# Performance work log

Measured on AMD Instinct MI355X. Metric: run time of the kernel, lower is better.

The kernel has to match this reference:

```python
import jax, jax.numpy as jnp
import numpy as np
import math

D_MODEL = 1024
NUM_HEADS = 16
D_K = D_MODEL // NUM_HEADS  # 64
B, S = 4, 2048


def setup_inputs() -> dict:
    key = jax.random.key(0)
    ks = jax.random.split(key, 9)
    sc = 1.0 / math.sqrt(D_MODEL)
    return {
        "x": jax.random.normal(ks[0], (B, S, D_MODEL), jnp.float32),
        "Wq": jax.random.normal(ks[1], (D_MODEL, D_MODEL), jnp.float32) * sc,
        "bq": jax.random.normal(ks[2], (D_MODEL,), jnp.float32) * 0.01,
        "Wk": jax.random.normal(ks[3], (D_MODEL, D_MODEL), jnp.float32) * sc,
        "bk": jax.random.normal(ks[4], (D_MODEL,), jnp.float32) * 0.01,
        "Wv": jax.random.normal(ks[5], (D_MODEL, D_MODEL), jnp.float32) * sc,
        "bv": jax.random.normal(ks[6], (D_MODEL,), jnp.float32) * 0.01,
        "Wo": jax.random.normal(ks[7], (D_MODEL, D_MODEL), jnp.float32) * sc,
        "bo": jax.random.normal(ks[8], (D_MODEL,), jnp.float32) * 0.01,
    }


def reference(x, Wq, bq, Wk, bk, Wv, bv, Wo, bo):
    b, s, d = x.shape
    # Linear projections (torch Linear: x @ W.T + b)
    Q = x @ Wq.T + bq
    K = x @ Wk.T + bk
    V = x @ Wv.T + bv
    # [b, s, h*d_k] -> [b, h, s, d_k]
    split = lambda t: t.reshape(b, s, NUM_HEADS, D_K).transpose(0, 2, 1, 3)
    Q, K, V = split(Q), split(K), split(V)
    # Causal mask: query i can attend to keys j <= i
    seq = jnp.arange(s)
    causal = seq[:, None] >= seq[None, :]  # [s, s]
    # Scaled dot-product attention
    scores = jnp.einsum('bhqd,bhkd->bhqk', Q, K) / math.sqrt(D_K)
    scores = jnp.where(causal, scores, -jnp.inf)
    weights = jax.nn.softmax(scores, axis=-1)
    attn = jnp.einsum('bhqk,bhkd->bhqd', weights, V)
    # [b, h, s, d_v] -> [b, s, h*d_v]
    attn = attn.transpose(0, 2, 1, 3).reshape(b, s, NUM_HEADS * D_K)
    return attn @ Wo.T + bo
```

## Files before the change

kernel.cpp:

```cpp
#include <hip/hip_runtime.h>
#include <hip/hip_bf16.h>


typedef unsigned short u16;
typedef unsigned int u32;
typedef __attribute__((ext_vector_type(2))) unsigned int uint2v;
typedef __attribute__((ext_vector_type(4))) unsigned int uint4v;
typedef __attribute__((ext_vector_type(4))) short short4v;
typedef __attribute__((ext_vector_type(8))) short short8;
typedef __attribute__((ext_vector_type(4))) float f32x4;
typedef __attribute__((ext_vector_type(16))) float f32x16;

#define KDIM   1024
#define S_LEN  2048
#define NHEADS 16
#define DK     64
#define NEG_BIG (-30000.0f)
#define QSCALE 0.18033688011112043f

__device__ __forceinline__ u16 f2bf(float f) {
  unsigned u = __float_as_uint(f);
  return (u16)((u + 0x7FFFu + ((u >> 16) & 1u)) >> 16);
}
__device__ __forceinline__ u32 pkbf(float a, float b) {
  u32 ua = __float_as_uint(a) + 0x8000u;
  u32 ub = __float_as_uint(b) + 0x8000u;
  return __builtin_amdgcn_perm(ub, ua, 0x07060302u);
}
__device__ __forceinline__ void gl_lds16(const u16* g, u16* l) {
  __builtin_amdgcn_global_load_lds((const __attribute__((address_space(1))) void*)g,
                                   (__attribute__((address_space(3))) void*)l, 16, 0, 0);
}

__global__ __launch_bounds__(256) void cvt_kernel(
    const float* __restrict__ x,  const float* __restrict__ Wq,
    const float* __restrict__ Wk, const float* __restrict__ Wv,
    u16* __restrict__ xb, u16* __restrict__ wqb,
    u16* __restrict__ wkb, u16* __restrict__ wvb) {
  const int NX = 2097152, NW = 262144;
  const int total = NX + 3 * NW;
  for (int i = blockIdx.x * 256 + threadIdx.x; i < total; i += gridDim.x * 256) {
    const float* src; u16* dst; int off;
    if (i < NX)               { src = x;  dst = xb;  off = i; }
    else if (i < NX + NW)     { src = Wq; dst = wqb; off = i - NX; }
    else if (i < NX + 2 * NW) { src = Wk; dst = wkb; off = i - NX - NW; }
    else                      { src = Wv; dst = wvb; off = i - NX - 2 * NW; }
    f32x4 v = *(const f32x4*)(src + (size_t)off * 4);
    short4v o;
    o[0] = (short)f2bf(v[0]); o[1] = (short)f2bf(v[1]);
    o[2] = (short)f2bf(v[2]); o[3] = (short)f2bf(v[3]);
    *(short4v*)(dst + (size_t)off * 4) = o;
  }
}

__global__ __launch_bounds__(256) void cvt_wo(const float* __restrict__ W,
                                              u16* __restrict__ out) {
  const int i = blockIdx.x * 256 + threadIdx.x;
  f32x4 v = *(const f32x4*)(W + (size_t)i * 4);
  short4v o;
  o[0] = (short)f2bf(v[0]); o[1] = (short)f2bf(v[1]);
  o[2] = (short)f2bf(v[2]); o[3] = (short)f2bf(v[3]);
  *(short4v*)(out + (size_t)i * 4) = o;
}

template <int MODE>
__device__ __forceinline__ void gemm_body(const u16* __restrict__ A,
                                          const u16* __restrict__ B,
                                          const float* __restrict__ bias,
                                          void* __restrict__ outv) {
  extern __shared__ __align__(16) u16 smem[];
  u16* As0 = smem;
  u16* As1 = smem + 4096;
  u16* Bs0 = smem + 8192;
  u16* Bs1 = smem + 12288;
  const int tid = threadIdx.x;
  const int wave = tid >> 6, lane = tid & 63;
  const int quad = lane >> 4, l16 = lane & 15;
  const int wy = wave >> 1, wx = wave & 1;
  const int m0 = blockIdx.x * 128, n0 = blockIdx.y * 128;

  f32x4 acc[4][4];
#pragma unroll
  for (int i = 0; i < 4; i++)
#pragma unroll
    for (int j = 0; j < 4; j++) acc[i][j] = (f32x4){0.f, 0.f, 0.f, 0.f};

  const int srow = wave * 16 + (lane >> 2);
  const int scol = (lane & 3) * 8;
  const u16* gA0 = A + (size_t)(m0 + srow) * KDIM + scol;
  const u16* gA1 = gA0 + (size_t)64 * KDIM;
  const u16* gB0 = B + (size_t)(n0 + srow) * KDIM + scol;
  const u16* gB1 = gB0 + (size_t)64 * KDIM;
  const int soff = srow * 32 + scol;

  for (int k = 0; k < KDIM; k += 64) {
    __syncthreads();
    gl_lds16(gA0 + k,      &As0[soff]);
    gl_lds16(gA0 + k + 32, &As1[soff]);
    gl_lds16(gA1 + k,      &As0[soff + 2048]);
    gl_lds16(gA1 + k + 32, &As1[soff + 2048]);
    gl_lds16(gB0 + k,      &Bs0[soff]);
    gl_lds16(gB0 + k + 32, &Bs1[soff]);
    gl_lds16(gB1 + k,      &Bs0[soff + 2048]);
    gl_lds16(gB1 + k + 32, &Bs1[soff + 2048]);
    __syncthreads();
#pragma unroll
    for (int h = 0; h < 2; h++) {
      const u16* Ap = h ? As1 : As0;
      const u16* Bp = h ? Bs1 : Bs0;
      short8 af[4], bfr[4];
#pragma unroll
      for (int i = 0; i < 4; i++)
        af[i] = *(const short8*)&Ap[(wy * 64 + i * 16 + l16) * 32 + quad * 8];
#pragma unroll
      for (int j = 0; j < 4; j++)
        bfr[j] = *(const short8*)&Bp[(wx * 64 + j * 16 + l16) * 32 + quad * 8];
#pragma unroll
      for (int i = 0; i < 4; i++)
#pragma unroll
        for (int j = 0; j < 4; j++) {
          if (MODE == 2)
            acc[i][j] = __builtin_amdgcn_mfma_f32_16x16x32_bf16(af[i], bfr[j], acc[i][j], 0, 0, 0);
          else
            acc[i][j] = __builtin_amdgcn_mfma_f32_16x16x32_bf16(bfr[j], af[i], acc[i][j], 0, 0, 0);
        }
    }
  }

  if (MODE == 0 || MODE == 1) {
#pragma unroll
    for (int j = 0; j < 4; j++) {
      const int colb = n0 + wx * 64 + j * 16 + quad * 4;
      const int h = colb >> 6, d0 = colb & 63;
      const f32x4 bv4 = *(const f32x4*)&bias[colb];
#pragma unroll
      for (int i = 0; i < 4; i++) {
        const int row = m0 + wy * 64 + i * 16 + l16;
        const int b = row >> 11, s = row & 2047;
        float v0 = acc[i][j][0] + bv4[0], v1 = acc[i][j][1] + bv4[1];
        float v2 = acc[i][j][2] + bv4[2], v3 = acc[i][j][3] + bv4[3];
        if (MODE == 0) { v0 *= QSCALE; v1 *= QSCALE; v2 *= QSCALE; v3 *= QSCALE; }
        uint2v pk = {pkbf(v0, v1), pkbf(v2, v3)};
        if (MODE == 0) {
          *(uint2v*)&((u16*)outv)[(((size_t)(b * NHEADS + h)) * S_LEN + s) * DK + d0] = pk;
        } else {
          *(uint2v*)&((u16*)outv)[((((size_t)(b * NHEADS + h)) * 32 + (s >> 6)) * 8 +
                                   (d0 >> 3)) * 512 + (s & 63) * 8 + (d0 & 7)] = pk;
        }
      }
    }
  } else if (MODE == 2) {
#pragma unroll
    for (int j = 0; j < 4; j++) {
      const int col = n0 + wx * 64 + j * 16 + l16;
      const int h = col >> 6, d = col & 63;
      const float bvs = bias[col];
#pragma unroll
      for (int i = 0; i < 4; i++) {
        const int rowb = m0 + wy * 64 + i * 16 + quad * 4;
        const int b = rowb >> 11, s0 = rowb & 2047;
        uint2v pk = {pkbf(acc[i][j][0] + bvs, acc[i][j][1] + bvs),
                     pkbf(acc[i][j][2] + bvs, acc[i][j][3] + bvs)};
        *(uint2v*)&((u16*)outv)[((((size_t)(b * NHEADS + h)) * 32 + (s0 >> 6)) * 8 +
                                 ((s0 >> 3) & 7)) * 512 + (size_t)d * 8 + (s0 & 7)] = pk;
      }
    }
  } else {
#pragma unroll
    for (int j = 0; j < 4; j++) {
      const int colb = n0 + wx * 64 + j * 16 + quad * 4;
      const f32x4 bv4 = *(const f32x4*)&bias[colb];
#pragma unroll
      for (int i = 0; i < 4; i++) {
        const int row = m0 + wy * 64 + i * 16 + l16;
        f32x4 v = {acc[i][j][0] + bv4[0], acc[i][j][1] + bv4[1],
                   acc[i][j][2] + bv4[2], acc[i][j][3] + bv4[3]};
        *(f32x4*)&((float*)outv)[(size_t)row * 1024 + colb] = v;
      }
    }
  }
}

__global__ __launch_bounds__(256) void qkv_gemm(
    const u16* __restrict__ xb,
    const u16* __restrict__ wqb, const float* __restrict__ bq,
    const u16* __restrict__ wkb, const float* __restrict__ bk,
    const u16* __restrict__ wvb, const float* __restrict__ bv,
    u16* __restrict__ qb, u16* __restrict__ kb, u16* __restrict__ vb) {
  if (blockIdx.z == 0)      gemm_body<0>(xb, wqb, bq, qb);
  else if (blockIdx.z == 1) gemm_body<1>(xb, wkb, bk, kb);
  else                      gemm_body<2>(xb, wvb, bv, vb);
}

__global__ __launch_bounds__(256) void out_gemm(const u16* __restrict__ A,
                                                const u16* __restrict__ wob,
                                                const float* __restrict__ bo,
                                                float* __restrict__ out) {
  gemm_body<3>(A, wob, bo, out);
}

__global__ __launch_bounds__(256) void attn_kernel(const u16* __restrict__ Qb,
                                                   const u16* __restrict__ Kb,
                                                   const u16* __restrict__ Vb,
                                                   u16* __restrict__ Ob) {
  __shared__ __align__(16) u16 Ks[2][8][512];
  __shared__ __align__(16) u16 Vs[2][8][512];
  const int bh = blockIdx.x;
  const int qt = (int)gridDim.y - 1 - (int)blockIdx.y;
  const int tid = threadIdx.x, wave = tid >> 6, lane = tid & 63;
  const int l32 = lane & 31, hi = lane >> 5;
  const u16* Qh = Qb + (size_t)bh * S_LEN * DK;
  const u16* Kg = Kb + (size_t)bh * S_LEN * DK;
  const u16* Vg = Vb + (size_t)bh * S_LEN * DK;
  const int qw = qt * 128 + wave * 32;
  const int qrow = qw + l32;

  short8 qf[4];
#pragma unroll
  for (int c = 0; c < 4; c++)
    qf[c] = *(const short8*)&Qh[(size_t)qrow * DK + c * 16 + hi * 8];

  short8 ones;
#pragma unroll
  for (int i = 0; i < 8; i++) ones[i] = (short)0x3F80;

  f32x16 zz;
#pragma unroll
  for (int i = 0; i < 16; i++) zz[i] = 0.f;
  f32x16 o0 = zz, o1 = zz, l_acc = zz;

  const int sg = wave * 2;
  const u16* srcK = Kg + sg * 512 + lane * 8;
  const u16* srcV = Vg + sg * 512 + lane * 8;
  u16* dstK0 = &Ks[0][sg][lane * 8];
  u16* dstK1 = &Ks[1][sg][lane * 8];
  u16* dstV0 = &Vs[0][sg][lane * 8];
  u16* dstV1 = &Vs[1][sg][lane * 8];

  for (int t = 0; t <= qt; ++t) {
    const size_t g0 = (size_t)(2 * t) * 4096, g1 = (size_t)(2 * t + 1) * 4096;
    __syncthreads();
    gl_lds16(srcK + g0, dstK0);        gl_lds16(srcK + g0 + 512, dstK0 + 512);
    gl_lds16(srcK + g1, dstK1);        gl_lds16(srcK + g1 + 512, dstK1 + 512);
    gl_lds16(srcV + g0, dstV0);        gl_lds16(srcV + g0 + 512, dstV0 + 512);
    gl_lds16(srcV + g1, dstV1);        gl_lds16(srcV + g1 + 512, dstV1 + 512);
    __syncthreads();

#pragma unroll
    for (int kb = 0; kb < 4; ++kb) {
      const int kbase = t * 128 + kb * 32;
      if (kbase > qw) break;

      f32x16 st = zz;
#pragma unroll
      for (int c = 0; c < 4; c++) {
        const short8 kf = *(const short8*)
            &Ks[kb >> 1][c * 2 + hi][((kb & 1) * 32 + l32) * 8];
        st = __builtin_amdgcn_mfma_f32_32x32x16_bf16(kf, qf[c], st, 0, 0, 0);
      }

      if (kbase == qw) {
#pragma unroll
        for (int r = 0; r < 16; r++) {
          const int ko = (r & 3) + 8 * (r >> 2) + 4 * hi;
          st[r] = (ko > l32) ? NEG_BIG : st[r];
        }
      }

      float e[16];
#pragma unroll
      for (int r = 0; r < 16; r++) e[r] = exp2f(st[r]);

      uint2v sA0 = __builtin_amdgcn_permlane32_swap(pkbf(e[0], e[1]),  pkbf(e[4], e[5]),  false, false);
      uint2v sB0 = __builtin_amdgcn_permlane32_swap(pkbf(e[2], e[3]),  pkbf(e[6], e[7]),  false, false);
      uint2v sA1 = __builtin_amdgcn_permlane32_swap(pkbf(e[8], e[9]),  pkbf(e[12], e[13]), false, false);
      uint2v sB1 = __builtin_amdgcn_permlane32_swap(pkbf(e[10], e[11]), pkbf(e[14], e[15]), false, false);
      union { uint4v u; short8 s; } p0, p1;
      p0.u = (uint4v){sA0[0], sB0[0], sA0[1], sB0[1]};
      p1.u = (uint4v){sA1[0], sB1[0], sA1[1], sB1[1]};
      const short8 pa0 = p0.s, pa1 = p1.s;

      l_acc = __builtin_amdgcn_mfma_f32_32x32x16_bf16(pa0, ones, l_acc, 0, 0, 0);
      l_acc = __builtin_amdgcn_mfma_f32_32x32x16_bf16(pa1, ones, l_acc, 0, 0, 0);

#pragma unroll
      for (int cc = 0; cc < 2; cc++) {
        const int kc = kb * 2 + cc;
        const short8 pa = cc ? pa1 : pa0;
        const short8 vf0 = *(const short8*)&Vs[kc >> 2][(kc & 3) * 2 + hi][l32 * 8];
        const short8 vf1 = *(const short8*)&Vs[kc >> 2][(kc & 3) * 2 + hi][(32 + l32) * 8];
        o0 = __builtin_amdgcn_mfma_f32_32x32x16_bf16(pa, vf0, o0, 0, 0, 0);
        o1 = __builtin_amdgcn_mfma_f32_32x32x16_bf16(pa, vf1, o1, 0, 0, 0);
      }
    }
  }

  const int b = bh >> 4, h = bh & 15;
#pragma unroll
  for (int r = 0; r < 16; r++) {
    const int s = qw + (r & 3) + 8 * (r >> 2) + 4 * hi;
    const float inv = __builtin_amdgcn_rcpf(l_acc[r]);
    const unsigned v0 = __float_as_uint(o0[r] * inv) + 0x8000u;
    const unsigned v1 = __float_as_uint(o1[r] * inv) + 0x8000u;
    u16* p = &Ob[((size_t)b * S_LEN + s) * 1024 + h * DK + l32];
    p[0]  = (u16)(v0 >> 16);
    p[32] = (u16)(v1 >> 16);
  }
}

extern "C" void kernel_launch(void* const* d_in, const int* in_sizes, int n_in,
                              void* d_out, int out_size, void* d_ws, size_t ws_size,
                              hipStream_t stream) {
  const float* x  = (const float*)d_in[0];
  const float* Wq = (const float*)d_in[1];
  const float* bq = (const float*)d_in[2];
  const float* Wk = (const float*)d_in[3];
  const float* bk = (const float*)d_in[4];
  const float* Wv = (const float*)d_in[5];
  const float* bv = (const float*)d_in[6];
  const float* Wo = (const float*)d_in[7];
  const float* bo = (const float*)d_in[8];

  u16* outh = (u16*)d_out;
  u16* wsh  = (u16*)d_ws;
  u16* qb  = outh;
  u16* xb  = outh + (size_t)8388608;
  u16* kb  = wsh;
  u16* vb  = wsh + (size_t)8388608;
  u16* ab  = wsh + (size_t)16777216;
  u16* wqb = ab;
  u16* wkb = wqb + (size_t)1048576;
  u16* wvb = wkb + (size_t)1048576;
  u16* wob = kb;

  cvt_kernel<<<dim3(2048), 256, 0, stream>>>(x, Wq, Wk, Wv, xb, wqb, wkb, wvb);
  qkv_gemm<<<dim3(64, 8, 3), 256, 32768, stream>>>(xb, wqb, bq, wkb, bk, wvb, bv, qb, kb, vb);
  attn_kernel<<<dim3(64, 16), 256, 0, stream>>>(qb, kb, vb, ab);
  cvt_wo<<<dim3(1024), 256, 0, stream>>>(Wo, wob);
  out_gemm<<<dim3(64, 8), 256, 32768, stream>>>(ab, wob, bo, (float*)d_out);
}
```

Baseline: 250.5 us.

## Double-buffer K/V tiles with prefetch overlap and raise MFMA wave priority

Changes the attention loop from loading 128-key tiles into both buffers and then computing, to a 64-key ping-pong scheme. The next tile's global-to-LDS load is issued before computing on the current one, with one barrier per iteration. It also wraps the MFMA sections in s_setprio to favour matrix issue across waves. The aim is to hide global load latency behind compute, at the cost of more loop iterations and barriers with smaller tiles. The single barrier placed after compute must ensure the prefetch into the other buffer does not race with readers.

```diff
diff --git a/kernel.cpp b/kernel.cpp
--- a/kernel.cpp
+++ b/kernel.cpp
@@ -232,32 +232,42 @@
   const int sg = wave * 2;
   const u16* srcK = Kg + sg * 512 + lane * 8;
   const u16* srcV = Vg + sg * 512 + lane * 8;
-  u16* dstK0 = &Ks[0][sg][lane * 8];
-  u16* dstK1 = &Ks[1][sg][lane * 8];
-  u16* dstV0 = &Vs[0][sg][lane * 8];
-  u16* dstV1 = &Vs[1][sg][lane * 8];
-
-  for (int t = 0; t <= qt; ++t) {
-    const size_t g0 = (size_t)(2 * t) * 4096, g1 = (size_t)(2 * t + 1) * 4096;
-    __syncthreads();
-    gl_lds16(srcK + g0, dstK0);        gl_lds16(srcK + g0 + 512, dstK0 + 512);
-    gl_lds16(srcK + g1, dstK1);        gl_lds16(srcK + g1 + 512, dstK1 + 512);
-    gl_lds16(srcV + g0, dstV0);        gl_lds16(srcV + g0 + 512, dstV0 + 512);
-    gl_lds16(srcV + g1, dstV1);        gl_lds16(srcV + g1 + 512, dstV1 + 512);
-    __syncthreads();
-
-#pragma unroll
-    for (int kb = 0; kb < 4; ++kb) {
-      const int kbase = t * 128 + kb * 32;
+  u16* dK[2] = {&Ks[0][sg][0] + lane * 8, &Ks[1][sg][0] + lane * 8};
+  u16* dV[2] = {&Vs[0][sg][0] + lane * 8, &Vs[1][sg][0] + lane * 8};
+
+  const int nt = 2 * qt + 2;
+
+  {
+    gl_lds16(srcK, dK[0]);  gl_lds16(srcK + 512, dK[0] + 512);
+    gl_lds16(srcV, dV[0]);  gl_lds16(srcV + 512, dV[0] + 512);
+  }
+  __syncthreads();
+
+  int cur = 0;
+  for (int t = 0; t < nt; ++t) {
+    if (t + 1 < nt) {
+      const size_t g = (size_t)(t + 1) * 4096;
+      const int nx = cur ^ 1;
+      gl_lds16(srcK + g, dK[nx]);  gl_lds16(srcK + g + 512, dK[nx] + 512);
+      gl_lds16(srcV + g, dV[nx]);  gl_lds16(srcV + g + 512, dV[nx] + 512);
+    }
+    const u16* Kc = &Ks[cur][0][0];
+    const u16* Vc = &Vs[cur][0][0];
+
+#pragma unroll
+    for (int kb = 0; kb < 2; ++kb) {
+      const int kbase = t * 64 + kb * 32;
       if (kbase > qw) break;
 
       f32x16 st = zz;
+      __builtin_amdgcn_s_setprio(1);
 #pragma unroll
       for (int c = 0; c < 4; c++) {
         const short8 kf = *(const short8*)
-            &Ks[kb >> 1][c * 2 + hi][((kb & 1) * 32 + l32) * 8];
+            &Kc[(size_t)(c * 2 + hi) * 512 + (kb * 32 + l32) * 8];
         st = __builtin_amdgcn_mfma_f32_32x32x16_bf16(kf, qf[c], st, 0, 0, 0);
       }
+      __builtin_amdgcn_s_setprio(0);
 
       if (kbase == qw) {
 #pragma unroll
@@ -280,6 +290,7 @@
       p1.u = (uint4v){sA1[0], sB1[0], sA1[1], sB1[1]};
       const short8 pa0 = p0.s, pa1 = p1.s;
 
+      __builtin_amdgcn_s_setprio(1);
       l_acc = __builtin_amdgcn_mfma_f32_32x32x16_bf16(pa0, ones, l_acc, 0, 0, 0);
       l_acc = __builtin_amdgcn_mfma_f32_32x32x16_bf16(pa1, ones, l_acc, 0, 0, 0);
 
@@ -287,12 +298,16 @@
       for (int cc = 0; cc < 2; cc++) {
         const int kc = kb * 2 + cc;
         const short8 pa = cc ? pa1 : pa0;
-        const short8 vf0 = *(const short8*)&Vs[kc >> 2][(kc & 3) * 2 + hi][l32 * 8];
-        const short8 vf1 = *(const short8*)&Vs[kc >> 2][(kc & 3) * 2 + hi][(32 + l32) * 8];
+        const short8 vf0 = *(const short8*)&Vc[(size_t)(kc * 2 + hi) * 512 + l32 * 8];
+        const short8 vf1 = *(const short8*)&Vc[(size_t)(kc * 2 + hi) * 512 + (32 + l32) * 8];
         o0 = __builtin_amdgcn_mfma_f32_32x32x16_bf16(pa, vf0, o0, 0, 0, 0);
         o1 = __builtin_amdgcn_mfma_f32_32x32x16_bf16(pa, vf1, o1, 0, 0, 0);
       }
-    }
+      __builtin_amdgcn_s_setprio(0);
+    }
+
+    if (t + 1 < nt) __syncthreads();
+    cur ^= 1;
   }
 
   const int b = bh >> 4, h = bh & 15;
```

After: 257.6 us. 1.03x slower.

## Split attention KV range across wave pairs and pair causal tiles per block

Applied to the files above, without the earlier changes.

The attention kernel now uses 512 threads: two wave groups each process half of every 128-key tile for the same 32 query rows, then combine partial outputs and row sums through LDS before writing. Each block also handles two query tiles (qt and 15-qt), which balances the causal triangle across blocks and halves the grid. The aim is more parallel MFMA work per CU and even per-block load. The cost is an extra LDS reduction and barriers per job, plus higher register pressure under the launch bound of 512 threads and min 4 blocks per CU.

```diff
diff --git a/kernel.cpp b/kernel.cpp
--- a/kernel.cpp
+++ b/kernel.cpp
@@ -199,112 +199,145 @@
   gemm_body<3>(A, wob, bo, out);
 }
 
-__global__ __launch_bounds__(256) void attn_kernel(const u16* __restrict__ Qb,
-                                                   const u16* __restrict__ Kb,
-                                                   const u16* __restrict__ Vb,
-                                                   u16* __restrict__ Ob) {
+__global__ __launch_bounds__(512, 4) void attn_kernel(const u16* __restrict__ Qb,
+                                                      const u16* __restrict__ Kb,
+                                                      const u16* __restrict__ Vb,
+                                                      u16* __restrict__ Ob) {
   __shared__ __align__(16) u16 Ks[2][8][512];
   __shared__ __align__(16) u16 Vs[2][8][512];
+  __shared__ float Lb[4][32];
   const int bh = blockIdx.x;
-  const int qt = (int)gridDim.y - 1 - (int)blockIdx.y;
   const int tid = threadIdx.x, wave = tid >> 6, lane = tid & 63;
   const int l32 = lane & 31, hi = lane >> 5;
+  const int sidx = wave & 3;
+  const int kh = wave >> 2;
   const u16* Qh = Qb + (size_t)bh * S_LEN * DK;
   const u16* Kg = Kb + (size_t)bh * S_LEN * DK;
   const u16* Vg = Vb + (size_t)bh * S_LEN * DK;
-  const int qw = qt * 128 + wave * 32;
-  const int qrow = qw + l32;
-
-  short8 qf[4];
-#pragma unroll
-  for (int c = 0; c < 4; c++)
-    qf[c] = *(const short8*)&Qh[(size_t)qrow * DK + c * 16 + hi * 8];
 
   short8 ones;
 #pragma unroll
   for (int i = 0; i < 8; i++) ones[i] = (short)0x3F80;
-
   f32x16 zz;
 #pragma unroll
   for (int i = 0; i < 16; i++) zz[i] = 0.f;
-  f32x16 o0 = zz, o1 = zz, l_acc = zz;
-
-  const int sg = wave * 2;
-  const u16* srcK = Kg + sg * 512 + lane * 8;
-  const u16* srcV = Vg + sg * 512 + lane * 8;
-  u16* dstK0 = &Ks[0][sg][lane * 8];
-  u16* dstK1 = &Ks[1][sg][lane * 8];
-  u16* dstV0 = &Vs[0][sg][lane * 8];
-  u16* dstV1 = &Vs[1][sg][lane * 8];
-
-  for (int t = 0; t <= qt; ++t) {
-    const size_t g0 = (size_t)(2 * t) * 4096, g1 = (size_t)(2 * t + 1) * 4096;
+
+  for (int job = 0; job < 2; ++job) {
+    const int qt = job ? (int)blockIdx.y : 15 - (int)blockIdx.y;
+    const int qw = qt * 128 + sidx * 32;
+    const int qrow = qw + l32;
+
+    short8 qf[4];
+#pragma unroll
+    for (int c = 0; c < 4; c++)
+      qf[c] = *(const short8*)&Qh[(size_t)qrow * DK + c * 16 + hi * 8];
+
+    f32x16 o0 = zz, o1 = zz, l_acc = zz;
+
+    for (int t = 0; t <= qt; ++t) {
+      __syncthreads();
+#pragma unroll
+      for (int j = 0; j < 4; ++j) {
+        const int i = wave * 4 + j;
+        const int ii = (i < 16) ? i : i - 16;
+        const int h = ii >> 3, sg = ii & 7;
+        const size_t goff = ((size_t)(2 * t + h)) * 4096 + sg * 512 + lane * 8;
+        if (i < 16) gl_lds16(Kg + goff, &Ks[h][sg][lane * 8]);
+        else        gl_lds16(Vg + goff, &Vs[h][sg][lane * 8]);
+      }
+      __syncthreads();
+
+#pragma unroll
+      for (int kb2 = 0; kb2 < 2; ++kb2) {
+        const int kb = kh * 2 + kb2;
+        const int kbase = t * 128 + kb * 32;
+        if (kbase > qw) break;
+
+        f32x16 st = zz;
+#pragma unroll
+        for (int c = 0; c < 4; c++) {
+          const short8 kf = *(const short8*)
+              &Ks[kb >> 1][c * 2 + hi][((kb & 1) * 32 + l32) * 8];
+          st = __builtin_amdgcn_mfma_f32_32x32x16_bf16(kf, qf[c], st, 0, 0, 0);
+        }
+
+        if (kbase == qw) {
+#pragma unroll
+          for (int r = 0; r < 16; r++) {
+            const int ko = (r & 3) + 8 * (r >> 2) + 4 * hi;
+            st[r] = (ko > l32) ? NEG_BIG : st[r];
+          }
+        }
+
+        float e[16];
+#pragma unroll
+        for (int r = 0; r < 16; r++) e[r] = exp2f(st[r]);
+
+        uint2v sA0 = __builtin_amdgcn_permlane32_swap(pkbf(e[0], e[1]),  pkbf(e[4], e[5]),  false, false);
+        uint2v sB0 = __builtin_amdgcn_permlane32_swap(pkbf(e[2], e[3]),  pkbf(e[6], e[7]),  false, false);
+        uint2v sA1 = __builtin_amdgcn_permlane32_swap(pkbf(e[8], e[9]),  pkbf(e[12], e[13]), false, false);
+        uint2v sB1 = __builtin_amdgcn_permlane32_swap(pkbf(e[10], e[11]), pkbf(e[14], e[15]), false, false);
+        union { uint4v u; short8 s; } p0, p1;
+        p0.u = (uint4v){sA0[0], sB0[0], sA0[1], sB0[1]};
+        p1.u = (uint4v){sA1[0], sB1[0], sA1[1], sB1[1]};
+        const short8 pa0 = p0.s, pa1 = p1.s;
+
+        l_acc = __builtin_amdgcn_mfma_f32_32x32x16_bf16(pa0, ones, l_acc, 0, 0, 0);
+        l_acc = __builtin_amdgcn_mfma_f32_32x32x16_bf16(pa1, ones, l_acc, 0, 0, 0);
+
+#pragma unroll
+        for (int cc = 0; cc < 2; cc++) {
+          const int kc = kb * 2 + cc;
+          const short8 pa = cc ? pa1 : pa0;
+          const short8 vf0 = *(const short8*)&Vs[kc >> 2][(kc & 3) * 2 + hi][l32 * 8];
+          const short8 vf1 = *(const short8*)&Vs[kc >> 2][(kc & 3) * 2 + hi][(32 + l32) * 8];
+          o0 = __builtin_amdgcn_mfma_f32_32x32x16_bf16(pa, vf0, o0, 0, 0, 0);
+          o1 = __builtin_amdgcn_mfma_f32_32x32x16_bf16(pa, vf1, o1, 0, 0, 0);
+        }
+      }
+    }
+
     __syncthreads();
-    gl_lds16(srcK + g0, dstK0);        gl_lds16(srcK + g0 + 512, dstK0 + 512);
-    gl_lds16(srcK + g1, dstK1);        gl_lds16(srcK + g1 + 512, dstK1 + 512);
-    gl_lds16(srcV + g0, dstV0);        gl_lds16(srcV + g0 + 512, dstV0 + 512);
-    gl_lds16(srcV + g1, dstV1);        gl_lds16(srcV + g1 + 512, dstV1 + 512);
+    float* C0 = (float*)&Ks[0][0][0];
+    float* C1 = (float*)&Vs[0][0][0];
+    const int cb = (sidx * 64 + lane) * 16;
+    if (kh == 1) {
+#pragma unroll
+      for (int q = 0; q < 4; q++) {
+        *(f32x4*)&C0[cb + q * 4] = (f32x4){o0[q*4+0], o0[q*4+1], o0[q*4+2], o0[q*4+3]};
+        *(f32x4*)&C1[cb + q * 4] = (f32x4){o1[q*4+0], o1[q*4+1], o1[q*4+2], o1[q*4+3]};
+      }
+      if (l32 == 0) {
+#pragma unroll
+        for (int r = 0; r < 16; r++)
+          Lb[sidx][(r & 3) + 8 * (r >> 2) + 4 * hi] = l_acc[r];
+      }
+    }
     __syncthreads();
-
-#pragma unroll
-    for (int kb = 0; kb < 4; ++kb) {
-      const int kbase = t * 128 + kb * 32;
-      if (kbase > qw) break;
-
-      f32x16 st = zz;
-#pragma unroll
-      for (int c = 0; c < 4; c++) {
-        const short8 kf = *(const short8*)
-            &Ks[kb >> 1][c * 2 + hi][((kb & 1) * 32 + l32) * 8];
-        st = __builtin_amdgcn_mfma_f32_32x32x16_bf16(kf, qf[c], st, 0, 0, 0);
-      }
-
-      if (kbase == qw) {
-#pragma unroll
-        for (int r = 0; r < 16; r++) {
-          const int ko = (r & 3) + 8 * (r >> 2) + 4 * hi;
-          st[r] = (ko > l32) ? NEG_BIG : st[r];
-        }
-      }
-
-      float e[16];
-#pragma unroll
-      for (int r = 0; r < 16; r++) e[r] = exp2f(st[r]);
-
-      uint2v sA0 = __builtin_amdgcn_permlane32_swap(pkbf(e[0], e[1]),  pkbf(e[4], e[5]),  false, false);
-      uint2v sB0 = __builtin_amdgcn_permlane32_swap(pkbf(e[2], e[3]),  pkbf(e[6], e[7]),  false, false);
-      uint2v sA1 = __builtin_amdgcn_permlane32_swap(pkbf(e[8], e[9]),  pkbf(e[12], e[13]), false, false);
-      uint2v sB1 = __builtin_amdgcn_permlane32_swap(pkbf(e[10], e[11]), pkbf(e[14], e[15]), false, false);
-      union { uint4v u; short8 s; } p0, p1;
-      p0.u = (uint4v){sA0[0], sB0[0], sA0[1], sB0[1]};
-      p1.u = (uint4v){sA1[0], sB1[0], sA1[1], sB1[1]};
-      const short8 pa0 = p0.s, pa1 = p1.s;
-
-      l_acc = __builtin_amdgcn_mfma_f32_32x32x16_bf16(pa0, ones, l_acc, 0, 0, 0);
-      l_acc = __builtin_amdgcn_mfma_f32_32x32x16_bf16(pa1, ones, l_acc, 0, 0, 0);
-
-#pragma unroll
-      for (int cc = 0; cc < 2; cc++) {
-        const int kc = kb * 2 + cc;
-        const short8 pa = cc ? pa1 : pa0;
-        const short8 vf0 = *(const short8*)&Vs[kc >> 2][(kc & 3) * 2 + hi][l32 * 8];
-        const short8 vf1 = *(const short8*)&Vs[kc >> 2][(kc & 3) * 2 + hi][(32 + l32) * 8];
-        o0 = __builtin_amdgcn_mfma_f32_32x32x16_bf16(pa, vf0, o0, 0, 0, 0);
-        o1 = __builtin_amdgcn_mfma_f32_32x32x16_bf16(pa, vf1, o1, 0, 0, 0);
-      }
-    }
-  }
-
-  const int b = bh >> 4, h = bh & 15;
-#pragma unroll
-  for (int r = 0; r < 16; r++) {
-    const int s = qw + (r & 3) + 8 * (r >> 2) + 4 * hi;
-    const float inv = __builtin_amdgcn_rcpf(l_acc[r]);
-    const unsigned v0 = __float_as_uint(o0[r] * inv) + 0x8000u;
-    const unsigned v1 = __float_as_uint(o1[r] * inv) + 0x8000u;
-    u16* p = &Ob[((size_t)b * S_LEN + s) * 1024 + h * DK + l32];
-    p[0]  = (u16)(v0 >> 16);
-    p[32] = (u16)(v1 >> 16);
+    if (kh == 0) {
+#pragma unroll
+      for (int q = 0; q < 4; q++) {
+        f32x4 a0 = *(const f32x4*)&C0[cb + q * 4];
+        f32x4 a1 = *(const f32x4*)&C1[cb + q * 4];
+        o0[q*4+0] += a0[0]; o0[q*4+1] += a0[1]; o0[q*4+2] += a0[2]; o0[q*4+3] += a0[3];
+        o1[q*4+0] += a1[0]; o1[q*4+1] += a1[1]; o1[q*4+2] += a1[2]; o1[q*4+3] += a1[3];
+      }
+#pragma unroll
+      for (int r = 0; r < 16; r++)
+        l_acc[r] += Lb[sidx][(r & 3) + 8 * (r >> 2) + 4 * hi];
+
+      const int b = bh >> 4, h = bh & 15;
+#pragma unroll
+      for (int r = 0; r < 16; r++) {
+        const int s = qw + (r & 3) + 8 * (r >> 2) + 4 * hi;
+        const float inv = __builtin_amdgcn_rcpf(l_acc[r]);
+        const unsigned v0 = __float_as_uint(o0[r] * inv) + 0x8000u;
+        const unsigned v1 = __float_as_uint(o1[r] * inv) + 0x8000u;
+        u16* p = &Ob[((size_t)b * S_LEN + s) * 1024 + h * DK + l32];
+        p[0]  = (u16)(v0 >> 16);
+        p[32] = (u16)(v1 >> 16);
+      }
+    }
   }
 }
 
@@ -335,7 +368,7 @@
 
   cvt_kernel<<<dim3(2048), 256, 0, stream>>>(x, Wq, Wk, Wv, xb, wqb, wkb, wvb);
   qkv_gemm<<<dim3(64, 8, 3), 256, 32768, stream>>>(xb, wqb, bq, wkb, bk, wvb, bv, qb, kb, vb);
-  attn_kernel<<<dim3(64, 16), 256, 0, stream>>>(qb, kb, vb, ab);
+  attn_kernel<<<dim3(64, 8), 512, 0, stream>>>(qb, kb, vb, ab);
   cvt_wo<<<dim3(1024), 256, 0, stream>>>(Wo, wob);
   out_gemm<<<dim3(64, 8), 256, 32768, stream>>>(ab, wob, bo, (float*)d_out);
 }
```

Measured after the change: 254.0 us. About the same (+1.4%).
